# Performance work log

Measured on AMD Instinct MI355X. Metric: run time of the kernel, lower is better.

Reference implementation:

```python
import jax, jax.numpy as jnp
import numpy as np

B = 1_000_000          # query points
D = 3                  # n_input_dims
N_LEVELS = 16
MIN_RES, MAX_RES = 16, 512
N_ENC = 2 ** 19        # max hashmap entries per level
N_EMBED = 2
INIT_SCALE = 1e-4
PRIMES = (1, 2654435761, 805459861)  # instant-ngp spatial-hash primes


def _resolutions():
    # Eq. 2/3 of instant-ngp: geometric growth from MIN_RES to MAX_RES
    growth = np.exp((np.log(MAX_RES) - np.log(MIN_RES)) / (N_LEVELS - 1))
    return [int(np.floor(MIN_RES * growth ** l)) for l in range(N_LEVELS)]

RES = _resolutions()
LEVEL_N_ENC = [min(r ** D, N_ENC) for r in RES]
LEVEL_HASH = [r ** D > N_ENC for r in RES]          # hash iff grid overflows table
CORNERS = np.stack(np.meshgrid(*([np.arange(2)] * D), indexing='ij'), -1).reshape(-1, D)  # (8,3)


def setup_inputs() -> dict:
    key = jax.random.key(0)
    ks = jax.random.split(key, N_LEVELS + 1)
    inp = {"x": jax.random.uniform(ks[0], (B, D), minval=-1.0, maxval=1.0, dtype=jnp.float32)}
    for l in range(N_LEVELS):
        inp[f"emb{l}"] = jax.random.uniform(
            ks[l + 1], (LEVEL_N_ENC[l], N_EMBED), minval=-INIT_SCALE, maxval=INIT_SCALE, dtype=jnp.float32
        )
    return inp


def _level_features(x, emb, res, n_enc, use_hash):
    # x: (B,3) in [-1,1] -> pixel coords, align_corners=False convention
    xp = (x + 1.0) * (res * 0.5) - 0.5
    x0 = jnp.floor(xp)
    t = xp - x0                                           # (B,3) fractional part
    ci = jnp.asarray(CORNERS, jnp.int32)                  # (8,3) corner offsets
    c = x0.astype(jnp.int32)[:, None, :] + ci[None]       # (B,8,3) corner coords
    off = jnp.asarray(CORNERS, xp.dtype)
    # trilinear weights: prod over dims of t or (1-t)
    w = jnp.prod(jnp.where(off[None] > 0, t[:, None, :], 1.0 - t[:, None, :]), axis=-1)  # (B,8)
    m = jnp.all((c >= 0) & (c < res), axis=-1)            # (B,8) zeros-padding mask
    if use_hash:
        cu = c.astype(jnp.uint32)
        h = cu[..., 0] * jnp.uint32(PRIMES[0])
        for d in range(1, D):
            h = h ^ (cu[..., d] * jnp.uint32(PRIMES[d]))
        ids = (h % jnp.uint32(n_enc)).astype(jnp.int32)
    else:
        # ravel index, x varies fastest ('xy' grid indexing)
        ids = (c[..., 0] + c[..., 1] * res + c[..., 2] * res * res) % n_enc
    ids = jnp.where(m, ids, 0)
    w = jnp.where(m, w, jnp.zeros_like(w))
    return jnp.sum(emb[ids] * w[..., None], axis=1)       # (B,E)


def reference(x, emb0, emb1, emb2, emb3, emb4, emb5, emb6, emb7,
              emb8, emb9, emb10, emb11, emb12, emb13, emb14, emb15):
    embs = [emb0, emb1, emb2, emb3, emb4, emb5, emb6, emb7,
            emb8, emb9, emb10, emb11, emb12, emb13, emb14, emb15]
    feats = [_level_features(x, embs[l], RES[l], LEVEL_N_ENC[l], LEVEL_HASH[l])
             for l in range(N_LEVELS)]
    return jnp.stack(feats, axis=1)  # (B, L, E)
```

## Files before the change

kernel.cpp:

```cpp
#include <hip/hip_runtime.h>
#include <stdint.h>


struct EmbPtrs { const float2* p[16]; };

constexpr int BLOCK  = 256;
constexpr int DBLOCK = 1024;
constexpr int L0N = 16*16*16;
constexpr int L1N = 20*20*20;
constexpr int NBINS = 32768;
constexpr int kRes[16] = {16,20,25,32,40,50,64,80,101,128,161,203,256,322,406,512};
constexpr uint32_t P1 = 2654435761u, P2 = 805459861u;
constexpr uint32_t HMASK = (1u << 19) - 1u;

struct Tri {
    int ix, iy, iz;
    float wx[2], wy[2], wz[2];
    bool vx[2], vy[2], vz[2];
};

template<int RES_>
__device__ __forceinline__ Tri tri_setup(float px, float py, float pz)
{
    Tri s;
    const float rh = (float)RES_ * 0.5f;
    const float xp = (px + 1.0f) * rh - 0.5f;
    const float yp = (py + 1.0f) * rh - 0.5f;
    const float zp = (pz + 1.0f) * rh - 0.5f;
    const float fx = floorf(xp), fy = floorf(yp), fz = floorf(zp);
    s.ix = (int)fx; s.iy = (int)fy; s.iz = (int)fz;
    const float tx = xp - fx, ty = yp - fy, tz = zp - fz;
    s.wx[0] = 1.0f - tx; s.wx[1] = tx;
    s.wy[0] = 1.0f - ty; s.wy[1] = ty;
    s.wz[0] = 1.0f - tz; s.wz[1] = tz;
    s.vx[0] = (s.ix   >= 0) && (s.ix   < RES_); s.vx[1] = (s.ix+1 >= 0) && (s.ix+1 < RES_);
    s.vy[0] = (s.iy   >= 0) && (s.iy   < RES_); s.vy[1] = (s.iy+1 >= 0) && (s.iy+1 < RES_);
    s.vz[0] = (s.iz   >= 0) && (s.iz   < RES_); s.vz[1] = (s.iz+1 >= 0) && (s.iz+1 < RES_);
    return s;
}

template<int RES_, typename PTR>
__device__ __forceinline__ float2 dense_feat(PTR tab, float px, float py, float pz)
{
    const Tri s = tri_setup<RES_>(px, py, pz);
    constexpr int r2 = RES_ * RES_;
    const int base = s.ix + s.iy * RES_ + s.iz * r2;
    float ax = 0.0f, ay = 0.0f;
#pragma unroll
    for (int k = 0; k < 2; ++k)
#pragma unroll
    for (int j = 0; j < 2; ++j)
#pragma unroll
    for (int i = 0; i < 2; ++i) {
        const bool v = s.vx[i] && s.vy[j] && s.vz[k];
        const uint32_t idx = v ? (uint32_t)(base + i + j*RES_ + k*r2) : 0u;
        const float w = v ? (s.wx[i]*s.wy[j]*s.wz[k]) : 0.0f;
        const float2 e = tab[idx];
        ax = fmaf(e.x, w, ax);
        ay = fmaf(e.y, w, ay);
    }
    return make_float2(ax, ay);
}

template<int RES_>
__device__ __forceinline__ float2 hash_feat(const float2* __restrict__ tab,
                                            float px, float py, float pz)
{
    const Tri s = tri_setup<RES_>(px, py, pz);
    const uint32_t hy0 = (uint32_t)s.iy * P1;
    const uint32_t hz0 = (uint32_t)s.iz * P2;
    const uint32_t hx[2] = {(uint32_t)s.ix, (uint32_t)s.ix + 1u};
    const uint32_t hy[2] = {hy0, hy0 + P1};
    const uint32_t hz[2] = {hz0, hz0 + P2};
    float ax = 0.0f, ay = 0.0f;
#pragma unroll
    for (int k = 0; k < 2; ++k)
#pragma unroll
    for (int j = 0; j < 2; ++j)
#pragma unroll
    for (int i = 0; i < 2; ++i) {
        const bool v = s.vx[i] && s.vy[j] && s.vz[k];
        uint32_t idx = (hx[i] ^ hy[j] ^ hz[k]) & HMASK;
        idx = v ? idx : 0u;
        const float w = v ? (s.wx[i]*s.wy[j]*s.wz[k]) : 0.0f;
        const float2 e = tab[idx];
        ax = fmaf(e.x, w, ax);
        ay = fmaf(e.y, w, ay);
    }
    return make_float2(ax, ay);
}

__device__ __forceinline__ uint32_t part1by2(uint32_t v)
{
    v = (v | (v << 16)) & 0x030000FFu;
    v = (v | (v << 8))  & 0x0300F00Fu;
    v = (v | (v << 4))  & 0x030C30C3u;
    v = (v | (v << 2))  & 0x09249249u;
    return v;
}

__device__ __forceinline__ uint32_t bin_of(float x, float y, float z)
{
    const int bx = min(max((int)((x + 1.0f) * 16.0f), 0), 31);
    const int by = min(max((int)((y + 1.0f) * 16.0f), 0), 31);
    const int bz = min(max((int)((z + 1.0f) * 16.0f), 0), 31);
    return part1by2((uint32_t)bx) | (part1by2((uint32_t)by) << 1) | (part1by2((uint32_t)bz) << 2);
}

__global__ __launch_bounds__(BLOCK) void hist_kernel(
    const float* __restrict__ x, uint32_t* __restrict__ hist, int n)
{
    const int b = blockIdx.x * BLOCK + threadIdx.x;
    if (b >= n) return;
    atomicAdd(&hist[bin_of(x[3*b+0], x[3*b+1], x[3*b+2])], 1u);
}

__global__ __launch_bounds__(1024) void scan_kernel(
    const uint32_t* __restrict__ hist, uint32_t* __restrict__ cursor)
{
    __shared__ uint32_t tot[1024];
    const int t = threadIdx.x;
    uint32_t v[32];
    uint32_t s = 0;
#pragma unroll
    for (int i = 0; i < 32; ++i) { v[i] = s; s += hist[t*32 + i]; }
    tot[t] = s;
    __syncthreads();
    for (int off = 1; off < 1024; off <<= 1) {
        const uint32_t y = (t >= off) ? tot[t - off] : 0u;
        __syncthreads();
        tot[t] += y;
        __syncthreads();
    }
    const uint32_t base = tot[t] - s;
#pragma unroll
    for (int i = 0; i < 32; ++i) cursor[t*32 + i] = base + v[i];
}

__global__ __launch_bounds__(BLOCK) void scatter_kernel(
    const float* __restrict__ x, uint32_t* __restrict__ cursor,
    float4* __restrict__ xs, int n)
{
    const int b = blockIdx.x * BLOCK + threadIdx.x;
    if (b >= n) return;
    const float px = x[3*b+0], py = x[3*b+1], pz = x[3*b+2];
    const uint32_t pos = atomicAdd(&cursor[bin_of(px, py, pz)], 1u);
    xs[pos] = make_float4(px, py, pz, __int_as_float(b));
}

__global__ __launch_bounds__(DBLOCK) void dense_kernel_binned(
    const float4* __restrict__ xs, EmbPtrs embs, float4* __restrict__ out, int n)
{
    __shared__ float2 lds0[L0N];
    __shared__ float2 lds1[L1N];
    {
        const float4* g0 = (const float4*)embs.p[0];
        const float4* g1 = (const float4*)embs.p[1];
        float4* s0 = (float4*)lds0;
        float4* s1 = (float4*)lds1;
#pragma unroll 2
        for (int i = threadIdx.x; i < L0N/2; i += DBLOCK) s0[i] = g0[i];
#pragma unroll 4
        for (int i = threadIdx.x; i < L1N/2; i += DBLOCK) s1[i] = g1[i];
    }
    __syncthreads();

    const int i = blockIdx.x * DBLOCK + threadIdx.x;
    if (i >= n) return;
    const float4 q = xs[i];
    const float px = q.x, py = q.y, pz = q.z;
    const int idx = __float_as_int(q.w);

    float2 f[8];
    f[0] = dense_feat<16>((const float2*)lds0, px, py, pz);
    f[1] = dense_feat<20>((const float2*)lds1, px, py, pz);
    f[2] = dense_feat<25>(embs.p[2], px, py, pz);
    f[3] = dense_feat<32>(embs.p[3], px, py, pz);
    f[4] = dense_feat<40>(embs.p[4], px, py, pz);
    f[5] = dense_feat<50>(embs.p[5], px, py, pz);
    f[6] = dense_feat<64>(embs.p[6], px, py, pz);
    f[7] = dense_feat<80>(embs.p[7], px, py, pz);

    float4* o = out + (size_t)idx * 8;
#pragma unroll
    for (int k = 0; k < 4; ++k)
        o[k] = make_float4(f[2*k].x, f[2*k].y, f[2*k+1].x, f[2*k+1].y);
}

__global__ __launch_bounds__(DBLOCK) void dense_kernel(
    const float* __restrict__ x, EmbPtrs embs, float4* __restrict__ out, int n)
{
    __shared__ float2 lds0[L0N];
    __shared__ float2 lds1[L1N];
    {
        const float4* g0 = (const float4*)embs.p[0];
        const float4* g1 = (const float4*)embs.p[1];
        float4* s0 = (float4*)lds0;
        float4* s1 = (float4*)lds1;
#pragma unroll 2
        for (int i = threadIdx.x; i < L0N/2; i += DBLOCK) s0[i] = g0[i];
#pragma unroll 4
        for (int i = threadIdx.x; i < L1N/2; i += DBLOCK) s1[i] = g1[i];
    }
    __syncthreads();

    const int b = blockIdx.x * DBLOCK + threadIdx.x;
    if (b >= n) return;
    const float px = x[3*b+0], py = x[3*b+1], pz = x[3*b+2];

    float2 f[8];
    f[0] = dense_feat<16>((const float2*)lds0, px, py, pz);
    f[1] = dense_feat<20>((const float2*)lds1, px, py, pz);
    f[2] = dense_feat<25>(embs.p[2], px, py, pz);
    f[3] = dense_feat<32>(embs.p[3], px, py, pz);
    f[4] = dense_feat<40>(embs.p[4], px, py, pz);
    f[5] = dense_feat<50>(embs.p[5], px, py, pz);
    f[6] = dense_feat<64>(embs.p[6], px, py, pz);
    f[7] = dense_feat<80>(embs.p[7], px, py, pz);

    float4* o = out + (size_t)b * 8;
#pragma unroll
    for (int i = 0; i < 4; ++i)
        o[i] = make_float4(f[2*i].x, f[2*i].y, f[2*i+1].x, f[2*i+1].y);
}

template<int L>
__global__ __launch_bounds__(BLOCK) void hash_level_kernel(
    const float* __restrict__ x, const float2* __restrict__ tab,
    float2* __restrict__ ws, int n)
{
    const int b = blockIdx.x * BLOCK + threadIdx.x;
    if (b >= n) return;
    ws[b] = hash_feat<kRes[L]>(tab, x[3*b+0], x[3*b+1], x[3*b+2]);
}

__global__ __launch_bounds__(BLOCK) void merge_kernel(
    const float2* __restrict__ ws, float4* __restrict__ out, int n)
{
    const int b = blockIdx.x * BLOCK + threadIdx.x;
    if (b >= n) return;
    float2 f[8];
#pragma unroll
    for (int l = 0; l < 8; ++l)
        f[l] = ws[(size_t)l * n + b];
    float4* o = out + (size_t)b * 8 + 4;
#pragma unroll
    for (int i = 0; i < 4; ++i)
        o[i] = make_float4(f[2*i].x, f[2*i].y, f[2*i+1].x, f[2*i+1].y);
}

__global__ __launch_bounds__(BLOCK) void fallback_kernel(
    const float* __restrict__ x, EmbPtrs embs, float4* __restrict__ out, int n)
{
    const int b = blockIdx.x * BLOCK + threadIdx.x;
    if (b >= n) return;
    const float px = x[3*b+0], py = x[3*b+1], pz = x[3*b+2];
    float2 f[16];
    f[0]  = dense_feat<16 >(embs.p[0],  px, py, pz);
    f[1]  = dense_feat<20 >(embs.p[1],  px, py, pz);
    f[2]  = dense_feat<25 >(embs.p[2],  px, py, pz);
    f[3]  = dense_feat<32 >(embs.p[3],  px, py, pz);
    f[4]  = dense_feat<40 >(embs.p[4],  px, py, pz);
    f[5]  = dense_feat<50 >(embs.p[5],  px, py, pz);
    f[6]  = dense_feat<64 >(embs.p[6],  px, py, pz);
    f[7]  = dense_feat<80 >(embs.p[7],  px, py, pz);
    f[8]  = hash_feat<101>(embs.p[8],  px, py, pz);
    f[9]  = hash_feat<128>(embs.p[9],  px, py, pz);
    f[10] = hash_feat<161>(embs.p[10], px, py, pz);
    f[11] = hash_feat<203>(embs.p[11], px, py, pz);
    f[12] = hash_feat<256>(embs.p[12], px, py, pz);
    f[13] = hash_feat<322>(embs.p[13], px, py, pz);
    f[14] = hash_feat<406>(embs.p[14], px, py, pz);
    f[15] = hash_feat<512>(embs.p[15], px, py, pz);
    float4* o = out + (size_t)b * 8;
#pragma unroll
    for (int i = 0; i < 8; ++i)
        o[i] = make_float4(f[2*i].x, f[2*i].y, f[2*i+1].x, f[2*i+1].y);
}

extern "C" void kernel_launch(void* const* d_in, const int* in_sizes, int n_in,
                              void* d_out, int out_size, void* d_ws, size_t ws_size,
                              hipStream_t stream) {
    const float* x = (const float*)d_in[0];
    EmbPtrs embs;
    for (int l = 0; l < 16; ++l) embs.p[l] = (const float2*)d_in[1 + l];
    const int n = in_sizes[0] / 3;
    const int grid  = (n + BLOCK - 1) / BLOCK;
    const int dgrid = (n + DBLOCK - 1) / DBLOCK;
    float4* out = (float4*)d_out;

    const size_t streamsB = (size_t)8 * (size_t)n * sizeof(float2);
    const size_t xsB      = (size_t)n * sizeof(float4);
    const size_t histB    = (size_t)NBINS * sizeof(uint32_t);
    const size_t needBin  = streamsB + xsB + 2 * histB;
    const size_t needR9   = streamsB;

    if (ws_size >= needBin) {
        float2*   ws     = (float2*)d_ws;
        float4*   xs     = (float4*)((char*)d_ws + streamsB);
        uint32_t* hist   = (uint32_t*)((char*)d_ws + streamsB + xsB);
        uint32_t* cursor = hist + NBINS;

        hipMemsetAsync(hist, 0, histB, stream);
        hist_kernel<<<grid, BLOCK, 0, stream>>>(x, hist, n);
        scan_kernel<<<1, 1024, 0, stream>>>(hist, cursor);
        scatter_kernel<<<grid, BLOCK, 0, stream>>>(x, cursor, xs, n);

        dense_kernel_binned<<<dgrid, DBLOCK, 0, stream>>>(xs, embs, out, n);
        hash_level_kernel< 8><<<grid, BLOCK, 0, stream>>>(x, embs.p[ 8], ws + 0*(size_t)n, n);
        hash_level_kernel< 9><<<grid, BLOCK, 0, stream>>>(x, embs.p[ 9], ws + 1*(size_t)n, n);
        hash_level_kernel<10><<<grid, BLOCK, 0, stream>>>(x, embs.p[10], ws + 2*(size_t)n, n);
        hash_level_kernel<11><<<grid, BLOCK, 0, stream>>>(x, embs.p[11], ws + 3*(size_t)n, n);
        hash_level_kernel<12><<<grid, BLOCK, 0, stream>>>(x, embs.p[12], ws + 4*(size_t)n, n);
        hash_level_kernel<13><<<grid, BLOCK, 0, stream>>>(x, embs.p[13], ws + 5*(size_t)n, n);
        hash_level_kernel<14><<<grid, BLOCK, 0, stream>>>(x, embs.p[14], ws + 6*(size_t)n, n);
        hash_level_kernel<15><<<grid, BLOCK, 0, stream>>>(x, embs.p[15], ws + 7*(size_t)n, n);
        merge_kernel<<<grid, BLOCK, 0, stream>>>(ws, out, n);
    } else if (ws_size >= needR9) {
        float2* ws = (float2*)d_ws;
        dense_kernel<<<dgrid, DBLOCK, 0, stream>>>(x, embs, out, n);
        hash_level_kernel< 8><<<grid, BLOCK, 0, stream>>>(x, embs.p[ 8], ws + 0*(size_t)n, n);
        hash_level_kernel< 9><<<grid, BLOCK, 0, stream>>>(x, embs.p[ 9], ws + 1*(size_t)n, n);
        hash_level_kernel<10><<<grid, BLOCK, 0, stream>>>(x, embs.p[10], ws + 2*(size_t)n, n);
        hash_level_kernel<11><<<grid, BLOCK, 0, stream>>>(x, embs.p[11], ws + 3*(size_t)n, n);
        hash_level_kernel<12><<<grid, BLOCK, 0, stream>>>(x, embs.p[12], ws + 4*(size_t)n, n);
        hash_level_kernel<13><<<grid, BLOCK, 0, stream>>>(x, embs.p[13], ws + 5*(size_t)n, n);
        hash_level_kernel<14><<<grid, BLOCK, 0, stream>>>(x, embs.p[14], ws + 6*(size_t)n, n);
        hash_level_kernel<15><<<grid, BLOCK, 0, stream>>>(x, embs.p[15], ws + 7*(size_t)n, n);
        merge_kernel<<<grid, BLOCK, 0, stream>>>(ws, out, n);
    } else {
        fallback_kernel<<<grid, BLOCK, 0, stream>>>(x, embs, out, n);
    }
}
```

Before: 645.0 us.

## Fuse per-level hash kernels into one binned kernel over spatially sorted points

Replaces the eight per-level hash kernels, which read unsorted x and wrote to a workspace, plus the merge kernel, with a single kernel. The new kernel reads the spatially binned points (xs) and evaluates all eight hash levels per point, writing directly to the output at the original index. This removes the workspace round trip and extra launches, and aims for better cache locality because neighbouring threads hit nearby table entries. The trade-off is that the per-level cache focus is lost, since all eight 4 MB tables are now active at once, and the dense_kernel fallback path is removed.

```diff
diff --git a/kernel.cpp b/kernel.cpp
--- a/kernel.cpp
+++ b/kernel.cpp
@@ -187,66 +187,29 @@
         o[k] = make_float4(f[2*k].x, f[2*k].y, f[2*k+1].x, f[2*k+1].y);
 }
 
-__global__ __launch_bounds__(DBLOCK) void dense_kernel(
-    const float* __restrict__ x, EmbPtrs embs, float4* __restrict__ out, int n)
-{
-    __shared__ float2 lds0[L0N];
-    __shared__ float2 lds1[L1N];
-    {
-        const float4* g0 = (const float4*)embs.p[0];
-        const float4* g1 = (const float4*)embs.p[1];
-        float4* s0 = (float4*)lds0;
-        float4* s1 = (float4*)lds1;
-#pragma unroll 2
-        for (int i = threadIdx.x; i < L0N/2; i += DBLOCK) s0[i] = g0[i];
-#pragma unroll 4
-        for (int i = threadIdx.x; i < L1N/2; i += DBLOCK) s1[i] = g1[i];
-    }
-    __syncthreads();
-
-    const int b = blockIdx.x * DBLOCK + threadIdx.x;
-    if (b >= n) return;
-    const float px = x[3*b+0], py = x[3*b+1], pz = x[3*b+2];
+__global__ __launch_bounds__(BLOCK) void hash_all_kernel(
+    const float4* __restrict__ xs, EmbPtrs embs, float4* __restrict__ out, int n)
+{
+    const int i = blockIdx.x * BLOCK + threadIdx.x;
+    if (i >= n) return;
+    const float4 q = xs[i];
+    const float px = q.x, py = q.y, pz = q.z;
+    const int idx = __float_as_int(q.w);
 
     float2 f[8];
-    f[0] = dense_feat<16>((const float2*)lds0, px, py, pz);
-    f[1] = dense_feat<20>((const float2*)lds1, px, py, pz);
-    f[2] = dense_feat<25>(embs.p[2], px, py, pz);
-    f[3] = dense_feat<32>(embs.p[3], px, py, pz);
-    f[4] = dense_feat<40>(embs.p[4], px, py, pz);
-    f[5] = dense_feat<50>(embs.p[5], px, py, pz);
-    f[6] = dense_feat<64>(embs.p[6], px, py, pz);
-    f[7] = dense_feat<80>(embs.p[7], px, py, pz);
-
-    float4* o = out + (size_t)b * 8;
-#pragma unroll
-    for (int i = 0; i < 4; ++i)
-        o[i] = make_float4(f[2*i].x, f[2*i].y, f[2*i+1].x, f[2*i+1].y);
-}
-
-template<int L>
-__global__ __launch_bounds__(BLOCK) void hash_level_kernel(
-    const float* __restrict__ x, const float2* __restrict__ tab,
-    float2* __restrict__ ws, int n)
-{
-    const int b = blockIdx.x * BLOCK + threadIdx.x;
-    if (b >= n) return;
-    ws[b] = hash_feat<kRes[L]>(tab, x[3*b+0], x[3*b+1], x[3*b+2]);
-}
-
-__global__ __launch_bounds__(BLOCK) void merge_kernel(
-    const float2* __restrict__ ws, float4* __restrict__ out, int n)
-{
-    const int b = blockIdx.x * BLOCK + threadIdx.x;
-    if (b >= n) return;
-    float2 f[8];
-#pragma unroll
-    for (int l = 0; l < 8; ++l)
-        f[l] = ws[(size_t)l * n + b];
-    float4* o = out + (size_t)b * 8 + 4;
-#pragma unroll
-    for (int i = 0; i < 4; ++i)
-        o[i] = make_float4(f[2*i].x, f[2*i].y, f[2*i+1].x, f[2*i+1].y);
+    f[0] = hash_feat<101>(embs.p[8],  px, py, pz);
+    f[1] = hash_feat<128>(embs.p[9],  px, py, pz);
+    f[2] = hash_feat<161>(embs.p[10], px, py, pz);
+    f[3] = hash_feat<203>(embs.p[11], px, py, pz);
+    f[4] = hash_feat<256>(embs.p[12], px, py, pz);
+    f[5] = hash_feat<322>(embs.p[13], px, py, pz);
+    f[6] = hash_feat<406>(embs.p[14], px, py, pz);
+    f[7] = hash_feat<512>(embs.p[15], px, py, pz);
+
+    float4* o = out + (size_t)idx * 8 + 4;
+#pragma unroll
+    for (int k = 0; k < 4; ++k)
+        o[k] = make_float4(f[2*k].x, f[2*k].y, f[2*k+1].x, f[2*k+1].y);
 }
 
 __global__ __launch_bounds__(BLOCK) void fallback_kernel(
@@ -289,16 +252,13 @@
     const int dgrid = (n + DBLOCK - 1) / DBLOCK;
     float4* out = (float4*)d_out;
 
-    const size_t streamsB = (size_t)8 * (size_t)n * sizeof(float2);
-    const size_t xsB      = (size_t)n * sizeof(float4);
-    const size_t histB    = (size_t)NBINS * sizeof(uint32_t);
-    const size_t needBin  = streamsB + xsB + 2 * histB;
-    const size_t needR9   = streamsB;
-
-    if (ws_size >= needBin) {
-        float2*   ws     = (float2*)d_ws;
-        float4*   xs     = (float4*)((char*)d_ws + streamsB);
-        uint32_t* hist   = (uint32_t*)((char*)d_ws + streamsB + xsB);
+    const size_t xsB   = (size_t)n * sizeof(float4);
+    const size_t histB = (size_t)NBINS * sizeof(uint32_t);
+    const size_t need  = xsB + 2 * histB;
+
+    if (ws_size >= need) {
+        float4*   xs     = (float4*)d_ws;
+        uint32_t* hist   = (uint32_t*)((char*)d_ws + xsB);
         uint32_t* cursor = hist + NBINS;
 
         hipMemsetAsync(hist, 0, histB, stream);
@@ -307,27 +267,7 @@
         scatter_kernel<<<grid, BLOCK, 0, stream>>>(x, cursor, xs, n);
 
         dense_kernel_binned<<<dgrid, DBLOCK, 0, stream>>>(xs, embs, out, n);
-        hash_level_kernel< 8><<<grid, BLOCK, 0, stream>>>(x, embs.p[ 8], ws + 0*(size_t)n, n);
-        hash_level_kernel< 9><<<grid, BLOCK, 0, stream>>>(x, embs.p[ 9], ws + 1*(size_t)n, n);
-        hash_level_kernel<10><<<grid, BLOCK, 0, stream>>>(x, embs.p[10], ws + 2*(size_t)n, n);
-        hash_level_kernel<11><<<grid, BLOCK, 0, stream>>>(x, embs.p[11], ws + 3*(size_t)n, n);
-        hash_level_kernel<12><<<grid, BLOCK, 0, stream>>>(x, embs.p[12], ws + 4*(size_t)n, n);
-        hash_level_kernel<13><<<grid, BLOCK, 0, stream>>>(x, embs.p[13], ws + 5*(size_t)n, n);
-        hash_level_kernel<14><<<grid, BLOCK, 0, stream>>>(x, embs.p[14], ws + 6*(size_t)n, n);
-        hash_level_kernel<15><<<grid, BLOCK, 0, stream>>>(x, embs.p[15], ws + 7*(size_t)n, n);
-        merge_kernel<<<grid, BLOCK, 0, stream>>>(ws, out, n);
-    } else if (ws_size >= needR9) {
-        float2* ws = (float2*)d_ws;
-        dense_kernel<<<dgrid, DBLOCK, 0, stream>>>(x, embs, out, n);
-        hash_level_kernel< 8><<<grid, BLOCK, 0, stream>>>(x, embs.p[ 8], ws + 0*(size_t)n, n);
-        hash_level_kernel< 9><<<grid, BLOCK, 0, stream>>>(x, embs.p[ 9], ws + 1*(size_t)n, n);
-        hash_level_kernel<10><<<grid, BLOCK, 0, stream>>>(x, embs.p[10], ws + 2*(size_t)n, n);
-        hash_level_kernel<11><<<grid, BLOCK, 0, stream>>>(x, embs.p[11], ws + 3*(size_t)n, n);
-        hash_level_kernel<12><<<grid, BLOCK, 0, stream>>>(x, embs.p[12], ws + 4*(size_t)n, n);
-        hash_level_kernel<13><<<grid, BLOCK, 0, stream>>>(x, embs.p[13], ws + 5*(size_t)n, n);
-        hash_level_kernel<14><<<grid, BLOCK, 0, stream>>>(x, embs.p[14], ws + 6*(size_t)n, n);
-        hash_level_kernel<15><<<grid, BLOCK, 0, stream>>>(x, embs.p[15], ws + 7*(size_t)n, n);
-        merge_kernel<<<grid, BLOCK, 0, stream>>>(ws, out, n);
+        hash_all_kernel<<<grid, BLOCK, 0, stream>>>(xs, embs, out, n);
     } else {
         fallback_kernel<<<grid, BLOCK, 0, stream>>>(x, embs, out, n);
     }
```

Measured after the change: 612.3 us. 5.1% less time.
